# Performance work log

Hardware: AMD Instinct MI355X
Metric: run time of the kernel (lower is better)

The kernel has to match this reference:

```python
import jax, jax.numpy as jnp
import numpy as np
from jax import lax

B, N = 4, 16384          # batch, points per cloud
NUM_GROUP = 1024         # FPS centers
GROUP_SIZE = 32          # KNN neighbors per center
ENC = 384                # encoder_channel
BN_EPS = 1e-5


def setup_inputs() -> dict:
    key = jax.random.key(0)
    ks = jax.random.split(key, 6)
    def rn(k, shape, scale=0.02):
        return jax.random.normal(k, shape, jnp.float32) * scale
    return {
        "xyz": jax.random.normal(ks[0], (B, N, 3), jnp.float32),
        # first_conv: Conv1d(3,128,1) -> BN(128) -> ReLU -> Conv1d(128,256,1)
        "w1": rn(ks[1], (128, 3)), "b1": jnp.zeros((128,), jnp.float32),
        "g1": jnp.ones((128,), jnp.float32), "be1": jnp.zeros((128,), jnp.float32),
        "m1": jnp.zeros((128,), jnp.float32), "v1": jnp.ones((128,), jnp.float32),
        "w2": rn(ks[2], (256, 128)), "b2": jnp.zeros((256,), jnp.float32),
        # second_conv: Conv1d(512,512,1) -> BN(512) -> ReLU -> Conv1d(512,384,1)
        "w3": rn(ks[3], (512, 512)), "b3": jnp.zeros((512,), jnp.float32),
        "g2": jnp.ones((512,), jnp.float32), "be2": jnp.zeros((512,), jnp.float32),
        "m2": jnp.zeros((512,), jnp.float32), "v2": jnp.ones((512,), jnp.float32),
        "w4": rn(ks[4], (ENC, 512)), "b4": jnp.zeros((ENC,), jnp.float32),
    }


def _bn(x, g, b, m, v):
    # eval-mode BatchNorm1d over channel (last) dim
    return (x - m) * (g / jnp.sqrt(v + BN_EPS)) + b


def _fps(xyz, npoint):
    # furthest point sampling; deterministic start at index 0
    b, n, _ = xyz.shape
    def step(carry, _):
        min_d, far = carry                              # [B,N], [B]
        c = xyz[jnp.arange(b), far]                     # [B,3]
        d = jnp.sum((xyz - c[:, None, :]) ** 2, -1)     # [B,N]
        min_d = jnp.minimum(min_d, d)
        nxt = jnp.argmax(min_d, -1).astype(jnp.int32)
        return (min_d, nxt), far
    init = (jnp.full((b, n), 1e10, jnp.float32), jnp.zeros((b,), jnp.int32))
    _, idx = lax.scan(step, init, None, length=npoint)  # [npoint, B]
    return idx.T                                        # [B, npoint]


def reference(xyz, w1, b1, g1, be1, m1, v1, w2, b2, w3, b3, g2, be2, m2, v2, w4, b4):
    bsz, n, _ = xyz.shape
    # ---- Group: FPS centers ----
    cidx = _fps(xyz, NUM_GROUP)                                   # [B,G] int32
    center = jax.vmap(lambda p, i: p[i])(xyz, cidx)               # [B,G,3]
    # ---- KNN (squared-distance top-k, ascending like sklearn) ----
    x2 = jnp.sum(xyz * xyz, -1)                                   # [B,N]
    c2 = jnp.sum(center * center, -1)                             # [B,G]
    d2 = c2[:, :, None] + x2[:, None, :] - 2.0 * jnp.einsum("bgc,bnc->bgn", center, xyz)
    _, idx = lax.top_k(-d2, GROUP_SIZE)                           # [B,G,k]
    # ---- neighborhood gather + center ----
    neigh = jax.vmap(lambda p, i: p[i])(xyz, idx)                 # [B,G,k,3]
    neigh = neigh - center[:, :, None, :]
    # ---- Encoder (PointNet-style, kernel-1 convs == per-point linears) ----
    g, k = NUM_GROUP, GROUP_SIZE
    x = neigh.reshape(bsz * g, k, 3)
    f = jax.nn.relu(_bn(x @ w1.T + b1, g1, be1, m1, v1)) @ w2.T + b2   # [BG,k,256]
    fg = jnp.max(f, axis=1, keepdims=True)                             # [BG,1,256]
    f = jnp.concatenate([jnp.broadcast_to(fg, f.shape), f], axis=-1)   # [BG,k,512]
    f = jax.nn.relu(_bn(f @ w3.T + b3, g2, be2, m2, v2)) @ w4.T + b4   # [BG,k,384]
    out = jnp.max(f, axis=1).reshape(bsz, g, ENC)                      # [B,G,384]
    return out
```

## Files before the change

kernel.cpp:

```cpp
#include <hip/hip_runtime.h>
#include <math.h>

#define BATCH   4
#define NPTS    16384
#define NGROUP  1024
#define GSIZE   32
#define ENCC    384
#define BN_EPS  1e-5f

typedef __bf16 bf16x8 __attribute__((ext_vector_type(8)));
typedef float  f32x4  __attribute__((ext_vector_type(4)));

#define DPP_AMAX(V, I, CTRL)                                                   \
  { int _vb = __float_as_int(V);                                               \
    int _ov = __builtin_amdgcn_update_dpp(_vb, _vb, (CTRL), 0xf, 0xf, false);  \
    int _oi = __builtin_amdgcn_update_dpp((I), (I), (CTRL), 0xf, 0xf, false);  \
    float _of = __int_as_float(_ov);                                           \
    if (_of > (V) || (_of == (V) && _oi < (I))) { (V) = _of; (I) = _oi; } }

#define DPP_AMIN(V, I, CTRL)                                                   \
  { int _vb = __float_as_int(V);                                               \
    int _ov = __builtin_amdgcn_update_dpp(_vb, _vb, (CTRL), 0xf, 0xf, false);  \
    int _oi = __builtin_amdgcn_update_dpp((I), (I), (CTRL), 0xf, 0xf, false);  \
    float _of = __int_as_float(_ov);                                           \
    if (_of < (V) || (_of == (V) && _oi < (I))) { (V) = _of; (I) = _oi; } }

__global__ __launch_bounds__(1024, 1)
void fps_kernel(const float* __restrict__ xyz, float4* __restrict__ centers4) {
  const int b   = blockIdx.x;
  const int tid = threadIdx.x;
  const float* base = xyz + (size_t)b * NPTS * 3;

  float px[16], py[16], pz[16], md[16];
#pragma unroll
  for (int t = 0; t < 16; ++t) {
    int i = tid + (t << 10);
    px[t] = base[i * 3 + 0];
    py[t] = base[i * 3 + 1];
    pz[t] = base[i * 3 + 2];
    md[t] = 1e10f;
  }

  __shared__ float s_val[2][16];
  __shared__ int   s_idx[2][16];

  int far = 0;
  for (int s = 0; s < NGROUP; ++s) {
    float cx = base[far * 3 + 0];
    float cy = base[far * 3 + 1];
    float cz = base[far * 3 + 2];
    if (tid == 0) {
      centers4[(size_t)b * NGROUP + s] =
          make_float4(cx, cy, cz, cx * cx + cy * cy + cz * cz);
    }

    float bv = -1.0f;
    int   bi = 0;
#pragma unroll
    for (int t = 0; t < 16; ++t) {
      float dx = px[t] - cx, dy = py[t] - cy, dz = pz[t] - cz;
      float d  = dx * dx + dy * dy + dz * dz;
      md[t] = fminf(md[t], d);
      if (md[t] > bv) { bv = md[t]; bi = tid + (t << 10); }
    }
    DPP_AMAX(bv, bi, 0x128)
    DPP_AMAX(bv, bi, 0x124)
    DPP_AMAX(bv, bi, 0x122)
    DPP_AMAX(bv, bi, 0x121)
    DPP_AMAX(bv, bi, 0x142)
    DPP_AMAX(bv, bi, 0x143)
    const int buf = s & 1;
    if ((tid & 63) == 63) { s_val[buf][tid >> 6] = bv; s_idx[buf][tid >> 6] = bi; }
    __syncthreads();
    float v = s_val[buf][tid & 15];
    int  ii = s_idx[buf][tid & 15];
    DPP_AMAX(v, ii, 0x128)
    DPP_AMAX(v, ii, 0x124)
    DPP_AMAX(v, ii, 0x122)
    DPP_AMAX(v, ii, 0x121)
    far = ii;
  }
}

__global__ __launch_bounds__(256)
void knn_kernel(const float* __restrict__ xyz, const float4* __restrict__ centers4,
                float* __restrict__ neigh) {
  const int gi  = blockIdx.x;
  const int b   = gi >> 10;
  const int tid = threadIdx.x;
  const float* base = xyz + (size_t)b * NPTS * 3;
  const float4 c4 = centers4[gi];

  float d[64];
  float cmv = 1e30f;
  int   cpos = 0;
#pragma unroll
  for (int t = 0; t < 64; ++t) {
    int i = tid + (t << 8);
    float x = base[i * 3 + 0], y = base[i * 3 + 1], z = base[i * 3 + 2];
    float x2  = x * x + y * y + z * z;
    float dt  = x * c4.x + y * c4.y + z * c4.z;
    float dd  = c4.w + x2 - 2.0f * dt;
    d[t] = dd;
    if (dd < cmv) { cmv = dd; cpos = t; }
  }

  __shared__ float s_cmv[256];
  __shared__ int   s_owner;
  __shared__ int   s_sel[GSIZE];
  s_cmv[tid] = cmv;
  __syncthreads();

  for (int r = 0; r < GSIZE; ++r) {
    if (tid < 64) {
      float v = s_cmv[tid]; int o = tid;
      float a = s_cmv[tid + 64];  if (a < v) { v = a; o = tid + 64; }
      float c = s_cmv[tid + 128]; if (c < v) { v = c; o = tid + 128; }
      float e = s_cmv[tid + 192]; if (e < v) { v = e; o = tid + 192; }
      DPP_AMIN(v, o, 0x128)
      DPP_AMIN(v, o, 0x124)
      DPP_AMIN(v, o, 0x122)
      DPP_AMIN(v, o, 0x121)
      DPP_AMIN(v, o, 0x142)
      DPP_AMIN(v, o, 0x143)
      if (tid == 63) s_owner = o;
    }
    __syncthreads();
    if (tid == s_owner) {
      s_sel[r] = tid + (cpos << 8);
#pragma unroll
      for (int t = 0; t < 64; ++t) if (t == cpos) d[t] = 1e30f;
      float nv = 1e30f; int np = 0;
#pragma unroll
      for (int t = 0; t < 64; ++t) { if (d[t] < nv) { nv = d[t]; np = t; } }
      cmv = nv; cpos = np;
      s_cmv[tid] = nv;
    }
    __syncthreads();
  }

  if (tid < GSIZE) {
    int i = s_sel[tid];
    float x = base[i * 3 + 0] - c4.x;
    float y = base[i * 3 + 1] - c4.y;
    float z = base[i * 3 + 2] - c4.z;
    size_t o = ((size_t)gi * GSIZE + tid) * 3;
    neigh[o + 0] = x; neigh[o + 1] = y; neigh[o + 2] = z;
  }
}

__global__ __launch_bounds__(256)
void prep_kernel(const float* __restrict__ w2f, const float* __restrict__ w3f,
                 const float* __restrict__ w4f, __bf16* __restrict__ bw2,
                 __bf16* __restrict__ bw3, __bf16* __restrict__ bw4) {
  int t = blockIdx.x * 256 + threadIdx.x;
  const float* src; __bf16* dst; int K, local;
  if (t < 4096)       { src = w2f; dst = bw2; K = 128; local = t; }
  else if (t < 36864) { src = w3f; dst = bw3; K = 512; local = t - 4096; }
  else                { src = w4f; dst = bw4; K = 512; local = t - 36864; }
  int lane = local & 63, ntks = local >> 6;
  int KS = K >> 5;
  int ks = ntks & (KS - 1), nt = ntks / KS;
  int ch = nt * 16 + (lane & 15);
  int k0 = ks * 32 + (lane >> 4) * 8;
  const float* s = src + (size_t)ch * K + k0;
  bf16x8 v;
#pragma unroll
  for (int j = 0; j < 8; ++j) v[j] = (__bf16)s[j];
  *reinterpret_cast<bf16x8*>(dst + (size_t)local * 8) = v;
}

#define R1S 136
#define HSS 520

__global__ __launch_bounds__(256, 2)
void encoder_kernel(const float* __restrict__ neigh,
                    const float* __restrict__ w1, const float* __restrict__ b1,
                    const float* __restrict__ g1, const float* __restrict__ be1,
                    const float* __restrict__ m1, const float* __restrict__ v1,
                    const __bf16* __restrict__ bw2, const float* __restrict__ b2,
                    const __bf16* __restrict__ bw3, const float* __restrict__ b3,
                    const float* __restrict__ g2, const float* __restrict__ be2,
                    const float* __restrict__ m2, const float* __restrict__ v2,
                    const __bf16* __restrict__ bw4, const float* __restrict__ b4,
                    float* __restrict__ out) {
  __shared__ __bf16 r1s[32][R1S];
  __shared__ __bf16 hs[32][HSS];
  __shared__ float  xs[32][4];
  __shared__ float  scr[4][388];

  const int gi = blockIdx.x, tid = threadIdx.x;
  const int w = tid >> 6, lane = tid & 63;
  const int lrow = lane & 15, lkg = lane >> 4;

  if (tid < GSIZE * 3) {
    int p = tid / 3, j = tid % 3;
    xs[p][j] = neigh[(size_t)gi * (GSIZE * 3) + tid];
  }
  __syncthreads();

  {
    const int c = tid & 127, ph2 = tid >> 7;
    float w10 = w1[c * 3 + 0], w11 = w1[c * 3 + 1], w12 = w1[c * 3 + 2];
    float b1c = b1[c], m1c = m1[c], be1c = be1[c];
    float s1c = g1[c] / sqrtf(v1[c] + BN_EPS);
#pragma unroll
    for (int i = 0; i < 16; ++i) {
      int p = i * 2 + ph2;
      float val = xs[p][0] * w10 + xs[p][1] * w11 + xs[p][2] * w12 + b1c;
      val = (val - m1c) * s1c + be1c;
      r1s[p][c] = (__bf16)fmaxf(val, 0.0f);
    }
  }
  __syncthreads();

  {
    bf16x8 afr[2][4];
#pragma unroll
    for (int mt = 0; mt < 2; ++mt)
#pragma unroll
      for (int ks = 0; ks < 4; ++ks)
        afr[mt][ks] = *reinterpret_cast<const bf16x8*>(&r1s[mt * 16 + lrow][ks * 32 + lkg * 8]);
#pragma unroll
    for (int t = 0; t < 4; ++t) {
      const int nt = w * 4 + t;
      f32x4 acc0 = {0.f, 0.f, 0.f, 0.f}, acc1 = {0.f, 0.f, 0.f, 0.f};
#pragma unroll
      for (int ks = 0; ks < 4; ++ks) {
        bf16x8 bfr = *reinterpret_cast<const bf16x8*>(bw2 + ((size_t)(nt * 4 + ks) * 64 + lane) * 8);
        acc0 = __builtin_amdgcn_mfma_f32_16x16x32_bf16(afr[0][ks], bfr, acc0, 0, 0, 0);
        acc1 = __builtin_amdgcn_mfma_f32_16x16x32_bf16(afr[1][ks], bfr, acc1, 0, 0, 0);
      }
      const int ch = nt * 16 + lrow;
      const float b2c = b2[ch];
#pragma unroll
      for (int j = 0; j < 4; ++j) {
        hs[lkg * 4 + j][256 + ch]      = (__bf16)(acc0[j] + b2c);
        hs[16 + lkg * 4 + j][256 + ch] = (__bf16)(acc1[j] + b2c);
      }
    }
  }
  __syncthreads();

  {
    float m = -1e30f;
#pragma unroll
    for (int p = 0; p < 32; ++p) m = fmaxf(m, (float)hs[p][256 + tid]);
    __bf16 mb = (__bf16)m;
#pragma unroll
    for (int p = 0; p < 32; ++p) hs[p][tid] = mb;
  }
  __syncthreads();

  {
    f32x4 acc[8][2];
#pragma unroll
    for (int u = 0; u < 8; ++u) { acc[u][0] = {0.f,0.f,0.f,0.f}; acc[u][1] = {0.f,0.f,0.f,0.f}; }
#pragma unroll
    for (int chunk = 0; chunk < 2; ++chunk) {
      for (int ks = 0; ks < 16; ++ks) {
        bf16x8 a0 = *reinterpret_cast<const bf16x8*>(&hs[lrow][ks * 32 + lkg * 8]);
        bf16x8 a1 = *reinterpret_cast<const bf16x8*>(&hs[16 + lrow][ks * 32 + lkg * 8]);
#pragma unroll
        for (int t = 0; t < 4; ++t) {
          const int u = chunk * 4 + t;
          const int nt = w * 8 + u;
          bf16x8 bfr = *reinterpret_cast<const bf16x8*>(bw3 + ((size_t)(nt * 16 + ks) * 64 + lane) * 8);
          acc[u][0] = __builtin_amdgcn_mfma_f32_16x16x32_bf16(a0, bfr, acc[u][0], 0, 0, 0);
          acc[u][1] = __builtin_amdgcn_mfma_f32_16x16x32_bf16(a1, bfr, acc[u][1], 0, 0, 0);
        }
      }
    }
    __syncthreads();
#pragma unroll
    for (int u = 0; u < 8; ++u) {
      const int ch = (w * 8 + u) * 16 + lrow;
      const float sc = g2[ch] / sqrtf(v2[ch] + BN_EPS);
      const float mm = m2[ch], bb = be2[ch], b3c = b3[ch];
#pragma unroll
      for (int mt = 0; mt < 2; ++mt)
#pragma unroll
        for (int j = 0; j < 4; ++j) {
          float val = ((acc[u][mt][j] + b3c) - mm) * sc + bb;
          hs[mt * 16 + lkg * 4 + j][ch] = (__bf16)fmaxf(val, 0.0f);
        }
    }
  }
  __syncthreads();

  {
    f32x4 acc[6][2];
#pragma unroll
    for (int u = 0; u < 6; ++u) { acc[u][0] = {0.f,0.f,0.f,0.f}; acc[u][1] = {0.f,0.f,0.f,0.f}; }
#pragma unroll
    for (int chunk = 0; chunk < 2; ++chunk) {
      for (int ks = 0; ks < 16; ++ks) {
        bf16x8 a0 = *reinterpret_cast<const bf16x8*>(&hs[lrow][ks * 32 + lkg * 8]);
        bf16x8 a1 = *reinterpret_cast<const bf16x8*>(&hs[16 + lrow][ks * 32 + lkg * 8]);
#pragma unroll
        for (int t = 0; t < 3; ++t) {
          const int u = chunk * 3 + t;
          const int nt = w * 6 + u;
          bf16x8 bfr = *reinterpret_cast<const bf16x8*>(bw4 + ((size_t)(nt * 16 + ks) * 64 + lane) * 8);
          acc[u][0] = __builtin_amdgcn_mfma_f32_16x16x32_bf16(a0, bfr, acc[u][0], 0, 0, 0);
          acc[u][1] = __builtin_amdgcn_mfma_f32_16x16x32_bf16(a1, bfr, acc[u][1], 0, 0, 0);
        }
      }
    }
#pragma unroll
    for (int u = 0; u < 6; ++u) {
      const int ch = (w * 6 + u) * 16 + lrow;
      float pm = -1e30f;
#pragma unroll
      for (int mt = 0; mt < 2; ++mt)
#pragma unroll
        for (int j = 0; j < 4; ++j) pm = fmaxf(pm, acc[u][mt][j]);
      scr[lkg][ch] = pm;
    }
  }
  __syncthreads();

  {
    float r = fmaxf(fmaxf(scr[0][tid], scr[1][tid]), fmaxf(scr[2][tid], scr[3][tid]));
    out[(size_t)gi * ENCC + tid] = r + b4[tid];
    if (tid < 128) {
      int c2 = tid + 256;
      float r2 = fmaxf(fmaxf(scr[0][c2], scr[1][c2]), fmaxf(scr[2][c2], scr[3][c2]));
      out[(size_t)gi * ENCC + c2] = r2 + b4[c2];
    }
  }
}

extern "C" void kernel_launch(void* const* d_in, const int* in_sizes, int n_in,
                              void* d_out, int out_size, void* d_ws, size_t ws_size,
                              hipStream_t stream) {
  const float* xyz = (const float*)d_in[0];
  const float* w1  = (const float*)d_in[1];
  const float* b1  = (const float*)d_in[2];
  const float* g1  = (const float*)d_in[3];
  const float* be1 = (const float*)d_in[4];
  const float* m1  = (const float*)d_in[5];
  const float* v1  = (const float*)d_in[6];
  const float* w2  = (const float*)d_in[7];
  const float* b2  = (const float*)d_in[8];
  const float* w3  = (const float*)d_in[9];
  const float* b3  = (const float*)d_in[10];
  const float* g2  = (const float*)d_in[11];
  const float* be2 = (const float*)d_in[12];
  const float* m2  = (const float*)d_in[13];
  const float* v2  = (const float*)d_in[14];
  const float* w4  = (const float*)d_in[15];
  const float* b4  = (const float*)d_in[16];
  float* out = (float*)d_out;

  char* ws = (char*)d_ws;
  float4* centers4 = (float4*)ws;
  float*  neigh    = (float*)(ws + 65536);
  __bf16* bw2      = (__bf16*)(ws + 65536 + 1572864);
  __bf16* bw3      = (__bf16*)(ws + 65536 + 1572864 + 65536);
  __bf16* bw4      = (__bf16*)(ws + 65536 + 1572864 + 65536 + 524288);

  prep_kernel<<<240, 256, 0, stream>>>(w2, w3, w4, bw2, bw3, bw4);
  fps_kernel<<<BATCH, 1024, 0, stream>>>(xyz, centers4);
  knn_kernel<<<BATCH * NGROUP, 256, 0, stream>>>(xyz, centers4, neigh);
  encoder_kernel<<<BATCH * NGROUP, 256, 0, stream>>>(
      neigh, w1, b1, g1, be1, m1, v1, bw2, b2, bw3, b3, g2, be2, m2, v2, bw4, b4, out);
}
```

Measured before the change: 2.529 ms.

## Restructure FPS with packed FP32 math, 512 threads and split argmax reduction

The furthest-point-sampling kernel now runs with 512 threads, each owning 32 contiguous points loaded as float4 and held as packed float2 pairs. Distances are computed with v_pk_add/mul/fma instructions. The per-step argmax becomes a value-only max reduction followed by a second min-index reduction over the points that match the maximum. This removes the paired value/index DPP shuffles from the serial 1024-step loop and halves the wave count, at the cost of a second block barrier per step and more registers per thread.

```diff
diff --git a/kernel.cpp b/kernel.cpp
--- a/kernel.cpp
+++ b/kernel.cpp
@@ -10,13 +10,20 @@
 
 typedef __bf16 bf16x8 __attribute__((ext_vector_type(8)));
 typedef float  f32x4  __attribute__((ext_vector_type(4)));
-
-#define DPP_AMAX(V, I, CTRL)                                                   \
+typedef float  f32x2  __attribute__((ext_vector_type(2)));
+
+#define PK_ADD(d, a, b) asm("v_pk_add_f32 %0, %1, %2" : "=v"(d) : "v"(a), "v"(b));
+#define PK_MUL(d, a, b) asm("v_pk_mul_f32 %0, %1, %2" : "=v"(d) : "v"(a), "v"(b));
+#define PK_FMA(d, a, b, c) asm("v_pk_fma_f32 %0, %1, %2, %3" : "=v"(d) : "v"(a), "v"(b), "v"(c));
+
+#define DPP_FMAX(V, CTRL)                                                      \
   { int _vb = __float_as_int(V);                                               \
     int _ov = __builtin_amdgcn_update_dpp(_vb, _vb, (CTRL), 0xf, 0xf, false);  \
-    int _oi = __builtin_amdgcn_update_dpp((I), (I), (CTRL), 0xf, 0xf, false);  \
-    float _of = __int_as_float(_ov);                                           \
-    if (_of > (V) || (_of == (V) && _oi < (I))) { (V) = _of; (I) = _oi; } }
+    (V) = fmaxf((V), __int_as_float(_ov)); }
+
+#define DPP_IMIN(V, CTRL)                                                      \
+  { int _ov = __builtin_amdgcn_update_dpp((V), (V), (CTRL), 0xf, 0xf, false);  \
+    (V) = min((V), _ov); }
 
 #define DPP_AMIN(V, I, CTRL)                                                   \
   { int _vb = __float_as_int(V);                                               \
@@ -25,60 +32,85 @@
     float _of = __int_as_float(_ov);                                           \
     if (_of < (V) || (_of == (V) && _oi < (I))) { (V) = _of; (I) = _oi; } }
 
-__global__ __launch_bounds__(1024, 1)
+__global__ __launch_bounds__(512, 1)
 void fps_kernel(const float* __restrict__ xyz, float4* __restrict__ centers4) {
   const int b   = blockIdx.x;
   const int tid = threadIdx.x;
   const float* base = xyz + (size_t)b * NPTS * 3;
 
-  float px[16], py[16], pz[16], md[16];
-#pragma unroll
-  for (int t = 0; t < 16; ++t) {
-    int i = tid + (t << 10);
-    px[t] = base[i * 3 + 0];
-    py[t] = base[i * 3 + 1];
-    pz[t] = base[i * 3 + 2];
-    md[t] = 1e10f;
-  }
-
-  __shared__ float s_val[2][16];
-  __shared__ int   s_idx[2][16];
+  f32x2 X[16], Y[16], Z[16], M[16];
+  {
+    float bufv[96];
+    const float4* src = reinterpret_cast<const float4*>(base + (size_t)tid * 96);
+#pragma unroll
+    for (int q = 0; q < 24; ++q) {
+      float4 v = src[q];
+      bufv[q * 4 + 0] = v.x; bufv[q * 4 + 1] = v.y;
+      bufv[q * 4 + 2] = v.z; bufv[q * 4 + 3] = v.w;
+    }
+#pragma unroll
+    for (int j = 0; j < 16; ++j) {
+      X[j] = f32x2{bufv[6 * j + 0], bufv[6 * j + 3]};
+      Y[j] = f32x2{bufv[6 * j + 1], bufv[6 * j + 4]};
+      Z[j] = f32x2{bufv[6 * j + 2], bufv[6 * j + 5]};
+      M[j] = f32x2{1e10f, 1e10f};
+    }
+  }
+
+  __shared__ float s_v[8];
+  __shared__ int   s_i[8];
 
   int far = 0;
   for (int s = 0; s < NGROUP; ++s) {
-    float cx = base[far * 3 + 0];
-    float cy = base[far * 3 + 1];
-    float cz = base[far * 3 + 2];
+    const float cx = base[far * 3 + 0];
+    const float cy = base[far * 3 + 1];
+    const float cz = base[far * 3 + 2];
     if (tid == 0) {
       centers4[(size_t)b * NGROUP + s] =
           make_float4(cx, cy, cz, cx * cx + cy * cy + cz * cz);
     }
-
-    float bv = -1.0f;
-    int   bi = 0;
-#pragma unroll
-    for (int t = 0; t < 16; ++t) {
-      float dx = px[t] - cx, dy = py[t] - cy, dz = pz[t] - cz;
-      float d  = dx * dx + dy * dy + dz * dz;
-      md[t] = fminf(md[t], d);
-      if (md[t] > bv) { bv = md[t]; bi = tid + (t << 10); }
-    }
-    DPP_AMAX(bv, bi, 0x128)
-    DPP_AMAX(bv, bi, 0x124)
-    DPP_AMAX(bv, bi, 0x122)
-    DPP_AMAX(bv, bi, 0x121)
-    DPP_AMAX(bv, bi, 0x142)
-    DPP_AMAX(bv, bi, 0x143)
-    const int buf = s & 1;
-    if ((tid & 63) == 63) { s_val[buf][tid >> 6] = bv; s_idx[buf][tid >> 6] = bi; }
+    const f32x2 nx = {-cx, -cx}, ny = {-cy, -cy}, nz = {-cz, -cz};
+
+    f32x2 bv2 = {-1.0f, -1.0f};
+#pragma unroll
+    for (int j = 0; j < 16; ++j) {
+      f32x2 dx, dy, dz, dd;
+      PK_ADD(dx, X[j], nx)
+      PK_ADD(dy, Y[j], ny)
+      PK_ADD(dz, Z[j], nz)
+      PK_MUL(dd, dx, dx)
+      PK_FMA(dd, dy, dy, dd)
+      PK_FMA(dd, dz, dz, dd)
+      M[j].x = fminf(M[j].x, dd.x);
+      M[j].y = fminf(M[j].y, dd.y);
+      bv2.x = fmaxf(bv2.x, M[j].x);
+      bv2.y = fmaxf(bv2.y, M[j].y);
+    }
+
+    float bv = fmaxf(bv2.x, bv2.y);
+    DPP_FMAX(bv, 0x128) DPP_FMAX(bv, 0x124) DPP_FMAX(bv, 0x122)
+    DPP_FMAX(bv, 0x121) DPP_FMAX(bv, 0x142) DPP_FMAX(bv, 0x143)
+    if ((tid & 63) == 63) s_v[tid >> 6] = bv;
     __syncthreads();
-    float v = s_val[buf][tid & 15];
-    int  ii = s_idx[buf][tid & 15];
-    DPP_AMAX(v, ii, 0x128)
-    DPP_AMAX(v, ii, 0x124)
-    DPP_AMAX(v, ii, 0x122)
-    DPP_AMAX(v, ii, 0x121)
-    far = ii;
+    float gv = s_v[tid & 7];
+    DPP_FMAX(gv, 0x124) DPP_FMAX(gv, 0x122) DPP_FMAX(gv, 0x121)
+
+    const float wm = __int_as_float(__builtin_amdgcn_readlane(__float_as_int(bv), 63));
+    int cand = 0x7fffffff;
+    if (wm == gv) {
+#pragma unroll
+      for (int j = 0; j < 16; ++j) {
+        if (M[j].x == gv) cand = min(cand, (tid << 5) + 2 * j);
+        if (M[j].y == gv) cand = min(cand, (tid << 5) + 2 * j + 1);
+      }
+    }
+    DPP_IMIN(cand, 0x128) DPP_IMIN(cand, 0x124) DPP_IMIN(cand, 0x122)
+    DPP_IMIN(cand, 0x121) DPP_IMIN(cand, 0x142) DPP_IMIN(cand, 0x143)
+    if ((tid & 63) == 63) s_i[tid >> 6] = cand;
+    __syncthreads();
+    int gidx = s_i[tid & 7];
+    DPP_IMIN(gidx, 0x124) DPP_IMIN(gidx, 0x122) DPP_IMIN(gidx, 0x121)
+    far = gidx;
   }
 }
 
@@ -361,7 +393,7 @@
   __bf16* bw4      = (__bf16*)(ws + 65536 + 1572864 + 65536 + 524288);
 
   prep_kernel<<<240, 256, 0, stream>>>(w2, w3, w4, bw2, bw3, bw4);
-  fps_kernel<<<BATCH, 1024, 0, stream>>>(xyz, centers4);
+  fps_kernel<<<BATCH, 512, 0, stream>>>(xyz, centers4);
   knn_kernel<<<BATCH * NGROUP, 256, 0, stream>>>(xyz, centers4, neigh);
   encoder_kernel<<<BATCH * NGROUP, 256, 0, stream>>>(
       neigh, w1, b1, g1, be1, m1, v1, bw2, b2, bw3, b3, g2, be2, m2, v2, bw4, b4, out);
```

Result: faster. 2.112 ms (-16.5%).
